# Optimization experiments

Hardware: AMD Instinct MI355X
Metric: run time of the kernel (lower is better)

## Reference

```python
import jax, jax.numpy as jnp
import numpy as np

NUM_HEADS = 16


def setup_inputs() -> dict:
    key = jax.random.key(0)
    ks = jax.random.split(key, 8)
    B, S, D = 2, 2048, 1024
    q = jax.random.normal(ks[0], (B, S, D), dtype=jnp.float32)
    k = jax.random.normal(ks[1], (B, S, D), dtype=jnp.float32)
    v = jax.random.normal(ks[2], (B, S, D), dtype=jnp.float32)
    mask = jax.random.randint(ks[3], (1, 1, S, S), 0, 2, dtype=jnp.int32)
    sc = 1.0 / np.sqrt(D)
    wq = jax.random.normal(ks[4], (D, D), dtype=jnp.float32) * sc
    wk = jax.random.normal(ks[5], (D, D), dtype=jnp.float32) * sc
    wv = jax.random.normal(ks[6], (D, D), dtype=jnp.float32) * sc
    wout = jax.random.normal(ks[7], (D, D), dtype=jnp.float32) * sc
    return {"q": q, "k": k, "v": v, "mask": mask,
            "wq": wq, "wk": wk, "wv": wv, "wout": wout}


def reference(q, k, v, mask, wq, wk, wv, wout):
    B, S, D = q.shape
    H = NUM_HEADS
    hd = D // H

    def proj(x, w):
        # nn.Linear(bias=False): x @ w.T, then split heads -> [B,H,S,hd]
        return (x @ w.T).reshape(B, -1, H, hd).transpose(0, 2, 1, 3)

    qh, kh, vh = proj(q, wq), proj(k, wk), proj(v, wv)
    scale = jnp.asarray(hd, q.dtype) ** 0.5
    scores = jnp.einsum('bhqd,bhkd->bhqk', qh, kh) / scale  # [B,H,S,S]
    att = jax.nn.softmax(scores, axis=-1)
    # NOTE: original applies masked_fill AFTER softmax with value -1e-9
    att = jnp.where(mask == 0, jnp.asarray(-1e-9, att.dtype), att)
    out = jnp.einsum('bhqk,bhkd->bhqd', att, vh)  # [B,H,S,hd]
    out = out.transpose(0, 2, 1, 3).reshape(B, S, D)
    return out @ wout.T
```

## Files before the change

kernel.cpp:

```cpp
#include <hip/hip_runtime.h>
#include <stdint.h>


#define BATCH  2
#define S_LEN  2048
#define DMODEL 1024
#define NH     16
#define HD     64

typedef __bf16 bf16_t;
typedef short  short8 __attribute__((ext_vector_type(8)));
typedef float  f32x4  __attribute__((ext_vector_type(4)));

#define AS1 __attribute__((address_space(1)))
#define AS3 __attribute__((address_space(3)))

static constexpr size_t MB = (size_t)1 << 20;
static constexpr size_t WS_REQUIRED = 112 * MB;
#define OFF_XHI(z)  ((size_t)(z) * 16 * MB)
#define OFF_XLO(z)  (OFF_XHI(z) + 8 * MB)
#define OFF_WHI(z)  (48 * MB + (size_t)(z) * 4 * MB)
#define OFF_WLO(z)  (OFF_WHI(z) + 2 * MB)
#define OFF_PHI(z)  (64 * MB + (size_t)(z) * 16 * MB)
#define OFF_PLO(z)  (OFF_PHI(z) + 8 * MB)
#define OFF_OHI     ((size_t)0)
#define OFF_OLO     (8 * MB)
#define OFF_MASKB   (16 * MB)

__device__ __forceinline__ f32x4 mfma_bf16(short8 a, short8 b, f32x4 c) {
    return __builtin_amdgcn_mfma_f32_16x16x32_bf16(a, b, c, 0, 0, 0);
}

__device__ __forceinline__ short8 ld8(const bf16_t* p) {
    return *reinterpret_cast<const short8*>(p);
}

__global__ void cvt_split_kernel(const float* __restrict__ x,
                                 bf16_t* __restrict__ hi, bf16_t* __restrict__ lo,
                                 int n) {
    int i = (blockIdx.x * blockDim.x + threadIdx.x) * 4;
    if (i >= n) return;
    const float4 v = *reinterpret_cast<const float4*>(x + i);
    float s[4] = {v.x, v.y, v.z, v.w};
    ushort hbits[4], lbits[4];
#pragma unroll
    for (int j = 0; j < 4; j++) {
        bf16_t hh = (bf16_t)s[j];
        bf16_t ll = (bf16_t)(s[j] - (float)hh);
        hbits[j] = __builtin_bit_cast(ushort, hh);
        lbits[j] = __builtin_bit_cast(ushort, ll);
    }
    *reinterpret_cast<ushort4*>(hi + i) = ushort4{hbits[0], hbits[1], hbits[2], hbits[3]};
    *reinterpret_cast<ushort4*>(lo + i) = ushort4{lbits[0], lbits[1], lbits[2], lbits[3]};
}

__global__ void cvt_mask_kernel(const int* __restrict__ m, bf16_t* __restrict__ mb, int n) {
    int i = (blockIdx.x * blockDim.x + threadIdx.x) * 4;
    if (i >= n) return;
    const int4 v = *reinterpret_cast<const int4*>(m + i);
    int s[4] = {v.x, v.y, v.z, v.w};
    ushort b[4];
#pragma unroll
    for (int j = 0; j < 4; j++) {
        bf16_t t = (bf16_t)(s[j] ? 1.0f : 0.0f);
        b[j] = __builtin_bit_cast(ushort, t);
    }
    *reinterpret_cast<ushort4*>(mb + i) = ushort4{b[0], b[1], b[2], b[3]};
}

template <int FINAL>
__global__ __launch_bounds__(256, 2) void gemm_split_kernel(char* __restrict__ ws,
                                                            float* __restrict__ fout) {
    __shared__ __align__(16) bf16_t AsH[128 * 32];
    __shared__ __align__(16) bf16_t AsL[128 * 32];
    __shared__ __align__(16) bf16_t BsH[128 * 32];
    __shared__ __align__(16) bf16_t BsL[128 * 32];

    const int z = FINAL ? 3 : blockIdx.z;
    const bf16_t* Ahi = FINAL ? (const bf16_t*)(ws + OFF_OHI) : (const bf16_t*)(ws + OFF_XHI(z));
    const bf16_t* Alo = FINAL ? (const bf16_t*)(ws + OFF_OLO) : (const bf16_t*)(ws + OFF_XLO(z));
    const bf16_t* Bhi = (const bf16_t*)(ws + OFF_WHI(z));
    const bf16_t* Blo = (const bf16_t*)(ws + OFF_WLO(z));
    bf16_t* Ohi = FINAL ? nullptr : (bf16_t*)(ws + OFF_PHI(z));
    bf16_t* Olo = FINAL ? nullptr : (bf16_t*)(ws + OFF_PLO(z));
    const float scale = (!FINAL && z == 0) ? 0.18033688011112042f : 1.0f;

    const int tid = threadIdx.x;
    const int lane = tid & 63, w = tid >> 6;
    const int wr = w >> 1, wc = w & 1;
    const int fr = lane & 15, fg = lane >> 4;
    const int m0 = blockIdx.x * 128, n0 = blockIdx.y * 128;
    const int K = 1024;

    f32x4 acc[4][4];
#pragma unroll
    for (int i = 0; i < 4; i++)
#pragma unroll
        for (int j = 0; j < 4; j++) acc[i][j] = f32x4{0.f, 0.f, 0.f, 0.f};

    AS3 bf16_t* asAH = (AS3 bf16_t*)AsH;
    AS3 bf16_t* asAL = (AS3 bf16_t*)AsL;
    AS3 bf16_t* asBH = (AS3 bf16_t*)BsH;
    AS3 bf16_t* asBL = (AS3 bf16_t*)BsL;

#pragma unroll 1
    for (int ks = 0; ks < K; ks += 32) {
        __syncthreads();
#pragma unroll
        for (int i = 0; i < 2; i++) {
            const int c = i * 256 + tid;
            const int row = c >> 2;
            const int ce = (c & 3) * 8;
            const size_t gA = (size_t)(m0 + row) * K + ks + ce;
            const size_t gB = (size_t)(n0 + row) * K + ks + ce;
            const size_t d = (size_t)(i * 256 + w * 64) * 8;
            __builtin_amdgcn_global_load_lds((const AS1 void*)(Ahi + gA), (AS3 void*)(asAH + d), 16, 0, 0);
            __builtin_amdgcn_global_load_lds((const AS1 void*)(Alo + gA), (AS3 void*)(asAL + d), 16, 0, 0);
            __builtin_amdgcn_global_load_lds((const AS1 void*)(Bhi + gB), (AS3 void*)(asBH + d), 16, 0, 0);
            __builtin_amdgcn_global_load_lds((const AS1 void*)(Blo + gB), (AS3 void*)(asBL + d), 16, 0, 0);
        }
        __syncthreads();

        short8 afh[4], afl[4], bfh[4], bfl[4];
#pragma unroll
        for (int i = 0; i < 4; i++) {
            const int ao = (wr * 64 + i * 16 + fr) * 32 + fg * 8;
            const int bo = (wc * 64 + i * 16 + fr) * 32 + fg * 8;
            afh[i] = ld8(&AsH[ao]);
            afl[i] = ld8(&AsL[ao]);
            bfh[i] = ld8(&BsH[bo]);
            bfl[i] = ld8(&BsL[bo]);
        }
#pragma unroll
        for (int i = 0; i < 4; i++)
#pragma unroll
            for (int j = 0; j < 4; j++) {
                acc[i][j] = mfma_bf16(afh[i], bfh[j], acc[i][j]);
                acc[i][j] = mfma_bf16(afh[i], bfl[j], acc[i][j]);
                acc[i][j] = mfma_bf16(afl[i], bfh[j], acc[i][j]);
            }
    }

#pragma unroll
    for (int i = 0; i < 4; i++) {
#pragma unroll
        for (int j = 0; j < 4; j++) {
            const int ncol = n0 + wc * 64 + j * 16 + fr;
#pragma unroll
            for (int r = 0; r < 4; r++) {
                const int m = m0 + wr * 64 + i * 16 + fg * 4 + r;
                const float val = acc[i][j][r] * scale;
                if (FINAL) {
                    fout[(size_t)m * DMODEL + ncol] = val;
                } else {
                    const bf16_t h = (bf16_t)val;
                    const bf16_t l = (bf16_t)(val - (float)h);
                    const int b = m >> 11, s = m & (S_LEN - 1);
                    const int hh = ncol >> 6, d = ncol & (HD - 1);
                    size_t idx;
                    if (z == 2) idx = ((size_t)(b * NH + hh) * HD + d) * S_LEN + s;
                    else        idx = ((size_t)(b * NH + hh) * S_LEN + s) * HD + d;
                    Ohi[idx] = h;
                    Olo[idx] = l;
                }
            }
        }
    }
}

__global__ __launch_bounds__(256, 2) void attn_kernel(char* __restrict__ ws) {
    __shared__ __align__(16) bf16_t KsH[2][8 * 64 * 8];
    __shared__ __align__(16) bf16_t KsL[2][8 * 64 * 8];
    __shared__ __align__(16) bf16_t VsH[8 * 64 * 8];
    __shared__ __align__(16) bf16_t VsL[8 * 64 * 8];

    const bf16_t* Qhi = (const bf16_t*)(ws + OFF_PHI(0));
    const bf16_t* Qlo = (const bf16_t*)(ws + OFF_PLO(0));
    const bf16_t* Khi = (const bf16_t*)(ws + OFF_PHI(1));
    const bf16_t* Klo = (const bf16_t*)(ws + OFF_PLO(1));
    const bf16_t* Vhi = (const bf16_t*)(ws + OFF_PHI(2));
    const bf16_t* Vlo = (const bf16_t*)(ws + OFF_PLO(2));
    const bf16_t* Mb  = (const bf16_t*)(ws + OFF_MASKB);
    bf16_t* Ohi = (bf16_t*)(ws + OFF_OHI);
    bf16_t* Olo = (bf16_t*)(ws + OFF_OLO);

    const int tid = threadIdx.x, lane = tid & 63, w = tid >> 6;
    const int fr = lane & 15, fg = lane >> 4;
    const int bh = blockIdx.y;
    const int q0 = blockIdx.x * 128;
    const int qrow0 = q0 + w * 32 + fr;
    const size_t qkBase = (size_t)bh * S_LEN * HD;
    const size_t vtBase = (size_t)bh * HD * S_LEN;

    size_t kSrc[2], vSrc[2];
#pragma unroll
    for (int i = 0; i < 2; i++) {
        const int s = i * 256 + tid;
        const int l = s & 63, f = (s >> 6) & 7;
        const int sfr = l & 15, sfg = l >> 4;
        const int cf = f >> 1, kc = f & 1;
        const int r = (cf & 1) * 4 + (sfr & 3) + (sfr >> 2) * 8 + (cf >> 1) * 32;
        kSrc[i] = qkBase + (size_t)r * HD + kc * 32 + sfg * 8;
        vSrc[i] = vtBase + (size_t)((f >> 1) * 16 + sfr) * S_LEN + (f & 1) * 32 + sfg * 8;
    }

    short8 qh[2][2], ql[2][2];
#pragma unroll
    for (int mf = 0; mf < 2; mf++)
#pragma unroll
        for (int kc = 0; kc < 2; kc++) {
            const size_t off = qkBase + (size_t)(qrow0 + mf * 16) * HD + kc * 32 + fg * 8;
            qh[mf][kc] = ld8(Qhi + off);
            ql[mf][kc] = ld8(Qlo + off);
        }

    f32x4 acco[2][4];
#pragma unroll
    for (int mf = 0; mf < 2; mf++)
#pragma unroll
        for (int df = 0; df < 4; df++) acco[mf][df] = f32x4{0.f, 0.f, 0.f, 0.f};
    float mrun[2] = {-__builtin_inff(), -__builtin_inff()};
    float lrun[2] = {0.f, 0.f};

    const size_t mrowBase0 = (size_t)qrow0 * S_LEN;
    const size_t mrowBase1 = (size_t)(qrow0 + 16) * S_LEN;

#define STAGE_K(K0, BUF)                                                                           \
    {                                                                                              \
        _Pragma("unroll") for (int i = 0; i < 2; i++) {                                            \
            const size_t ko = kSrc[i] + (size_t)(K0) * HD;                                         \
            const size_t dst = (size_t)(i * 256 + w * 64) * 8;                                     \
            __builtin_amdgcn_global_load_lds((const AS1 void*)(Khi + ko),                          \
                                             (AS3 void*)((AS3 bf16_t*)KsH[BUF] + dst), 16, 0, 0);  \
            __builtin_amdgcn_global_load_lds((const AS1 void*)(Klo + ko),                          \
                                             (AS3 void*)((AS3 bf16_t*)KsL[BUF] + dst), 16, 0, 0);  \
        }                                                                                          \
    }
#define STAGE_V(K0)                                                                                \
    {                                                                                              \
        _Pragma("unroll") for (int i = 0; i < 2; i++) {                                            \
            const size_t vo = vSrc[i] + (K0);                                                      \
            const size_t dst = (size_t)(i * 256 + w * 64) * 8;                                     \
            __builtin_amdgcn_global_load_lds((const AS1 void*)(Vhi + vo),                          \
                                             (AS3 void*)((AS3 bf16_t*)VsH + dst), 16, 0, 0);       \
            __builtin_amdgcn_global_load_lds((const AS1 void*)(Vlo + vo),                          \
                                             (AS3 void*)((AS3 bf16_t*)VsL + dst), 16, 0, 0);       \
        }                                                                                          \
    }

    STAGE_K(0, 0)
    short8 mvCur[2][2], mvNxt[2][2];
    mvCur[0][0] = ld8(Mb + mrowBase0 + fg * 8);
    mvCur[0][1] = ld8(Mb + mrowBase0 + 32 + fg * 8);
    mvCur[1][0] = ld8(Mb + mrowBase1 + fg * 8);
    mvCur[1][1] = ld8(Mb + mrowBase1 + 32 + fg * 8);
#pragma unroll
    for (int mf = 0; mf < 2; mf++)
#pragma unroll
        for (int hh = 0; hh < 2; hh++) mvNxt[mf][hh] = mvCur[mf][hh];
    __syncthreads();

    int cur = 0;
#pragma unroll 1
    for (int k0 = 0; k0 < S_LEN; k0 += 64) {
        STAGE_V(k0)
        if (k0 + 64 < S_LEN) {
            STAGE_K(k0 + 64, cur ^ 1)
            mvNxt[0][0] = ld8(Mb + mrowBase0 + (k0 + 64) + fg * 8);
            mvNxt[0][1] = ld8(Mb + mrowBase0 + (k0 + 64) + 32 + fg * 8);
            mvNxt[1][0] = ld8(Mb + mrowBase1 + (k0 + 64) + fg * 8);
            mvNxt[1][1] = ld8(Mb + mrowBase1 + (k0 + 64) + 32 + fg * 8);
        }

        f32x4 sacc[2][4];
#pragma unroll
        for (int mf = 0; mf < 2; mf++)
#pragma unroll
            for (int cf = 0; cf < 4; cf++) sacc[mf][cf] = f32x4{0.f, 0.f, 0.f, 0.f};
        __builtin_amdgcn_s_setprio(1);
#pragma unroll
        for (int cf = 0; cf < 4; cf++) {
#pragma unroll
            for (int kc = 0; kc < 2; kc++) {
                const int fi = cf * 2 + kc;
                const short8 kh = ld8(&KsH[cur][(fi * 64 + lane) * 8]);
                const short8 kl = ld8(&KsL[cur][(fi * 64 + lane) * 8]);
#pragma unroll
                for (int mf = 0; mf < 2; mf++) {
                    sacc[mf][cf] = mfma_bf16(kh, qh[mf][kc], sacc[mf][cf]);
                    sacc[mf][cf] = mfma_bf16(kl, qh[mf][kc], sacc[mf][cf]);
                    sacc[mf][cf] = mfma_bf16(kh, ql[mf][kc], sacc[mf][cf]);
                }
            }
        }
        __builtin_amdgcn_s_setprio(0);

        float p[2][4][4];
#pragma unroll
        for (int mf = 0; mf < 2; mf++) {
            float mx = sacc[mf][0][0];
#pragma unroll
            for (int cf = 0; cf < 4; cf++)
#pragma unroll
                for (int r = 0; r < 4; r++) mx = fmaxf(mx, sacc[mf][cf][r]);
            mx = fmaxf(mx, __shfl_xor(mx, 16, 64));
            mx = fmaxf(mx, __shfl_xor(mx, 32, 64));
            if (!__all(mx <= mrun[mf] + 8.0f)) {
                const float mnew = fmaxf(mrun[mf], mx);
                const float alpha = exp2f(mrun[mf] - mnew);
                mrun[mf] = mnew;
                lrun[mf] *= alpha;
#pragma unroll
                for (int df = 0; df < 4; df++) acco[mf][df] *= alpha;
            }
            float psum = 0.f;
#pragma unroll
            for (int cf = 0; cf < 4; cf++)
#pragma unroll
                for (int r = 0; r < 4; r++) {
                    p[mf][cf][r] = exp2f(sacc[mf][cf][r] - mrun[mf]);
                    psum += p[mf][cf][r];
                }
            psum += __shfl_xor(psum, 16, 64);
            psum += __shfl_xor(psum, 32, 64);
            lrun[mf] += psum;
        }

        short8 phi[2][2], plo[2][2];
#pragma unroll
        for (int mf = 0; mf < 2; mf++)
#pragma unroll
            for (int kc2 = 0; kc2 < 2; kc2++)
#pragma unroll
                for (int j = 0; j < 8; j++) {
                    const int cf = kc2 * 2 + (j >> 2), r = j & 3;
                    const float mvf = (float)__builtin_bit_cast(
                        bf16_t, (ushort)(mvCur[mf][cf >> 1][(cf & 1) * 4 + r]));
                    const float pm = p[mf][cf][r] * mvf;
                    const bf16_t h = (bf16_t)pm;
                    const bf16_t l = (bf16_t)(pm - (float)h);
                    phi[mf][kc2][j] = __builtin_bit_cast(short, h);
                    plo[mf][kc2][j] = __builtin_bit_cast(short, l);
                }

        __syncthreads();

        __builtin_amdgcn_s_setprio(1);
#pragma unroll
        for (int kc2 = 0; kc2 < 2; kc2++) {
#pragma unroll
            for (int df = 0; df < 4; df++) {
                const int fi = df * 2 + kc2;
                const short8 vh = ld8(&VsH[(fi * 64 + lane) * 8]);
                const short8 vl = ld8(&VsL[(fi * 64 + lane) * 8]);
#pragma unroll
                for (int mf = 0; mf < 2; mf++) {
                    acco[mf][df] = mfma_bf16(vh, phi[mf][kc2], acco[mf][df]);
                    acco[mf][df] = mfma_bf16(vl, phi[mf][kc2], acco[mf][df]);
                    acco[mf][df] = mfma_bf16(vh, plo[mf][kc2], acco[mf][df]);
                }
            }
        }
        __builtin_amdgcn_s_setprio(0);

        __syncthreads();
#pragma unroll
        for (int mf = 0; mf < 2; mf++)
#pragma unroll
            for (int hh = 0; hh < 2; hh++) mvCur[mf][hh] = mvNxt[mf][hh];
        cur ^= 1;
    }
#undef STAGE_K
#undef STAGE_V

    const int b = bh >> 4, hh = bh & (NH - 1);
#pragma unroll
    for (int mf = 0; mf < 2; mf++) {
        const float inv = 1.0f / lrun[mf];
        const size_t obase = ((size_t)b * S_LEN + qrow0 + mf * 16) * DMODEL + hh * HD;
#pragma unroll
        for (int df = 0; df < 4; df++) {
#pragma unroll
            for (int r = 0; r < 4; r++) {
                const int d = df * 16 + fg * 4 + r;
                const float o = acco[mf][df][r] * inv;
                const bf16_t h = (bf16_t)o;
                Ohi[obase + d] = h;
                Olo[obase + d] = (bf16_t)(o - (float)h);
            }
        }
    }
}

extern "C" void kernel_launch(void* const* d_in, const int* in_sizes, int n_in,
                              void* d_out, int out_size, void* d_ws, size_t ws_size,
                              hipStream_t stream) {
    (void)in_sizes; (void)n_in; (void)out_size;
    if (ws_size < WS_REQUIRED) return;

    const float* q    = (const float*)d_in[0];
    const float* k    = (const float*)d_in[1];
    const float* v    = (const float*)d_in[2];
    const int*   mask = (const int*)  d_in[3];
    const float* wq   = (const float*)d_in[4];
    const float* wk   = (const float*)d_in[5];
    const float* wv   = (const float*)d_in[6];
    const float* wout = (const float*)d_in[7];
    char* ws = (char*)d_ws;
    float* out = (float*)d_out;

    const size_t nX = (size_t)BATCH * S_LEN * DMODEL;
    const size_t nW = (size_t)DMODEL * DMODEL;
    const size_t nM = (size_t)S_LEN * S_LEN;
    const dim3 blk(256);

    cvt_split_kernel<<<dim3(nX / 1024), blk, 0, stream>>>(q, (bf16_t*)(ws + OFF_XHI(0)), (bf16_t*)(ws + OFF_XLO(0)), (int)nX);
    cvt_split_kernel<<<dim3(nX / 1024), blk, 0, stream>>>(k, (bf16_t*)(ws + OFF_XHI(1)), (bf16_t*)(ws + OFF_XLO(1)), (int)nX);
    cvt_split_kernel<<<dim3(nX / 1024), blk, 0, stream>>>(v, (bf16_t*)(ws + OFF_XHI(2)), (bf16_t*)(ws + OFF_XLO(2)), (int)nX);
    cvt_split_kernel<<<dim3(nW / 1024), blk, 0, stream>>>(wq,   (bf16_t*)(ws + OFF_WHI(0)), (bf16_t*)(ws + OFF_WLO(0)), (int)nW);
    cvt_split_kernel<<<dim3(nW / 1024), blk, 0, stream>>>(wk,   (bf16_t*)(ws + OFF_WHI(1)), (bf16_t*)(ws + OFF_WLO(1)), (int)nW);
    cvt_split_kernel<<<dim3(nW / 1024), blk, 0, stream>>>(wv,   (bf16_t*)(ws + OFF_WHI(2)), (bf16_t*)(ws + OFF_WLO(2)), (int)nW);
    cvt_split_kernel<<<dim3(nW / 1024), blk, 0, stream>>>(wout, (bf16_t*)(ws + OFF_WHI(3)), (bf16_t*)(ws + OFF_WLO(3)), (int)nW);

    gemm_split_kernel<0><<<dim3(32, 8, 3), blk, 0, stream>>>(ws, nullptr);

    cvt_mask_kernel<<<dim3(nM / 1024), blk, 0, stream>>>(mask, (bf16_t*)(ws + OFF_MASKB), (int)nM);

    attn_kernel<<<dim3(S_LEN / 128, BATCH * NH), blk, 0, stream>>>(ws);

    gemm_split_kernel<1><<<dim3(32, 8, 1), blk, 0, stream>>>(ws, out);
}
```

Measured before the change: 419.3 us.

## Double-buffer split-bf16 GEMM LDS tiles and batch conversion launches

```diff
diff --git a/kernel.cpp b/kernel.cpp
--- a/kernel.cpp
+++ b/kernel.cpp
@@ -35,11 +35,10 @@
     return *reinterpret_cast<const short8*>(p);
 }
 
-__global__ void cvt_split_kernel(const float* __restrict__ x,
-                                 bf16_t* __restrict__ hi, bf16_t* __restrict__ lo,
-                                 int n) {
-    int i = (blockIdx.x * blockDim.x + threadIdx.x) * 4;
-    if (i >= n) return;
+__device__ __forceinline__ void cvt_split_body(const float* __restrict__ x,
+                                               bf16_t* __restrict__ hi,
+                                               bf16_t* __restrict__ lo) {
+    const int i = (blockIdx.x * blockDim.x + threadIdx.x) * 4;
     const float4 v = *reinterpret_cast<const float4*>(x + i);
     float s[4] = {v.x, v.y, v.z, v.w};
     ushort hbits[4], lbits[4];
@@ -52,6 +51,21 @@
     }
     *reinterpret_cast<ushort4*>(hi + i) = ushort4{hbits[0], hbits[1], hbits[2], hbits[3]};
     *reinterpret_cast<ushort4*>(lo + i) = ushort4{lbits[0], lbits[1], lbits[2], lbits[3]};
+}
+
+__global__ void cvt_qkv_kernel(const float* __restrict__ q, const float* __restrict__ k,
+                               const float* __restrict__ v, char* __restrict__ ws) {
+    const int z = blockIdx.y;
+    const float* src = (z == 0) ? q : (z == 1) ? k : v;
+    cvt_split_body(src, (bf16_t*)(ws + OFF_XHI(z)), (bf16_t*)(ws + OFF_XLO(z)));
+}
+
+__global__ void cvt_w_kernel(const float* __restrict__ wq, const float* __restrict__ wk,
+                             const float* __restrict__ wv, const float* __restrict__ wout,
+                             char* __restrict__ ws) {
+    const int z = blockIdx.y;
+    const float* src = (z == 0) ? wq : (z == 1) ? wk : (z == 2) ? wv : wout;
+    cvt_split_body(src, (bf16_t*)(ws + OFF_WHI(z)), (bf16_t*)(ws + OFF_WLO(z)));
 }
 
 __global__ void cvt_mask_kernel(const int* __restrict__ m, bf16_t* __restrict__ mb, int n) {
@@ -71,10 +85,10 @@
 template <int FINAL>
 __global__ __launch_bounds__(256, 2) void gemm_split_kernel(char* __restrict__ ws,
                                                             float* __restrict__ fout) {
-    __shared__ __align__(16) bf16_t AsH[128 * 32];
-    __shared__ __align__(16) bf16_t AsL[128 * 32];
-    __shared__ __align__(16) bf16_t BsH[128 * 32];
-    __shared__ __align__(16) bf16_t BsL[128 * 32];
+    __shared__ __align__(16) bf16_t AsH[2][128 * 32];
+    __shared__ __align__(16) bf16_t AsL[2][128 * 32];
+    __shared__ __align__(16) bf16_t BsH[2][128 * 32];
+    __shared__ __align__(16) bf16_t BsL[2][128 * 32];
 
     const int z = FINAL ? 3 : blockIdx.z;
     const bf16_t* Ahi = FINAL ? (const bf16_t*)(ws + OFF_OHI) : (const bf16_t*)(ws + OFF_XHI(z));
@@ -98,39 +112,52 @@
 #pragma unroll
         for (int j = 0; j < 4; j++) acc[i][j] = f32x4{0.f, 0.f, 0.f, 0.f};
 
-    AS3 bf16_t* asAH = (AS3 bf16_t*)AsH;
-    AS3 bf16_t* asAL = (AS3 bf16_t*)AsL;
-    AS3 bf16_t* asBH = (AS3 bf16_t*)BsH;
-    AS3 bf16_t* asBL = (AS3 bf16_t*)BsL;
-
+    size_t gAoff[2], gBoff[2], ldst[2];
+#pragma unroll
+    for (int i = 0; i < 2; i++) {
+        const int c = i * 256 + tid;
+        const int row = c >> 2;
+        const int ce = (c & 3) * 8;
+        gAoff[i] = (size_t)(m0 + row) * K + ce;
+        gBoff[i] = (size_t)(n0 + row) * K + ce;
+        ldst[i] = (size_t)(i * 256 + w * 64) * 8;
+    }
+
+#define GSTAGE(KS, BUF)                                                                            \
+    {                                                                                              \
+        _Pragma("unroll") for (int i = 0; i < 2; i++) {                                            \
+            const size_t gA = gAoff[i] + (KS);                                                     \
+            const size_t gB = gBoff[i] + (KS);                                                     \
+            __builtin_amdgcn_global_load_lds((const AS1 void*)(Ahi + gA),                          \
+                                             (AS3 void*)((AS3 bf16_t*)AsH[BUF] + ldst[i]), 16, 0, 0); \
+            __builtin_amdgcn_global_load_lds((const AS1 void*)(Alo + gA),                          \
+                                             (AS3 void*)((AS3 bf16_t*)AsL[BUF] + ldst[i]), 16, 0, 0); \
+            __builtin_amdgcn_global_load_lds((const AS1 void*)(Bhi + gB),                          \
+                                             (AS3 void*)((AS3 bf16_t*)BsH[BUF] + ldst[i]), 16, 0, 0); \
+            __builtin_amdgcn_global_load_lds((const AS1 void*)(Blo + gB),                          \
+                                             (AS3 void*)((AS3 bf16_t*)BsL[BUF] + ldst[i]), 16, 0, 0); \
+        }                                                                                          \
+    }
+
+    GSTAGE(0, 0)
+    __syncthreads();
+
+    int cur = 0;
 #pragma unroll 1
     for (int ks = 0; ks < K; ks += 32) {
-        __syncthreads();
-#pragma unroll
-        for (int i = 0; i < 2; i++) {
-            const int c = i * 256 + tid;
-            const int row = c >> 2;
-            const int ce = (c & 3) * 8;
-            const size_t gA = (size_t)(m0 + row) * K + ks + ce;
-            const size_t gB = (size_t)(n0 + row) * K + ks + ce;
-            const size_t d = (size_t)(i * 256 + w * 64) * 8;
-            __builtin_amdgcn_global_load_lds((const AS1 void*)(Ahi + gA), (AS3 void*)(asAH + d), 16, 0, 0);
-            __builtin_amdgcn_global_load_lds((const AS1 void*)(Alo + gA), (AS3 void*)(asAL + d), 16, 0, 0);
-            __builtin_amdgcn_global_load_lds((const AS1 void*)(Bhi + gB), (AS3 void*)(asBH + d), 16, 0, 0);
-            __builtin_amdgcn_global_load_lds((const AS1 void*)(Blo + gB), (AS3 void*)(asBL + d), 16, 0, 0);
-        }
-        __syncthreads();
+        if (ks + 32 < K) GSTAGE(ks + 32, cur ^ 1)
 
         short8 afh[4], afl[4], bfh[4], bfl[4];
 #pragma unroll
         for (int i = 0; i < 4; i++) {
             const int ao = (wr * 64 + i * 16 + fr) * 32 + fg * 8;
             const int bo = (wc * 64 + i * 16 + fr) * 32 + fg * 8;
-            afh[i] = ld8(&AsH[ao]);
-            afl[i] = ld8(&AsL[ao]);
-            bfh[i] = ld8(&BsH[bo]);
-            bfl[i] = ld8(&BsL[bo]);
-        }
+            afh[i] = ld8(&AsH[cur][ao]);
+            afl[i] = ld8(&AsL[cur][ao]);
+            bfh[i] = ld8(&BsH[cur][bo]);
+            bfl[i] = ld8(&BsL[cur][bo]);
+        }
+        __builtin_amdgcn_s_setprio(1);
 #pragma unroll
         for (int i = 0; i < 4; i++)
 #pragma unroll
@@ -139,7 +166,12 @@
                 acc[i][j] = mfma_bf16(afh[i], bfl[j], acc[i][j]);
                 acc[i][j] = mfma_bf16(afl[i], bfh[j], acc[i][j]);
             }
-    }
+        __builtin_amdgcn_s_setprio(0);
+
+        __syncthreads();
+        cur ^= 1;
+    }
+#undef GSTAGE
 
 #pragma unroll
     for (int i = 0; i < 4; i++) {
@@ -414,13 +446,8 @@
     const size_t nM = (size_t)S_LEN * S_LEN;
     const dim3 blk(256);
 
-    cvt_split_kernel<<<dim3(nX / 1024), blk, 0, stream>>>(q, (bf16_t*)(ws + OFF_XHI(0)), (bf16_t*)(ws + OFF_XLO(0)), (int)nX);
-    cvt_split_kernel<<<dim3(nX / 1024), blk, 0, stream>>>(k, (bf16_t*)(ws + OFF_XHI(1)), (bf16_t*)(ws + OFF_XLO(1)), (int)nX);
-    cvt_split_kernel<<<dim3(nX / 1024), blk, 0, stream>>>(v, (bf16_t*)(ws + OFF_XHI(2)), (bf16_t*)(ws + OFF_XLO(2)), (int)nX);
-    cvt_split_kernel<<<dim3(nW / 1024), blk, 0, stream>>>(wq,   (bf16_t*)(ws + OFF_WHI(0)), (bf16_t*)(ws + OFF_WLO(0)), (int)nW);
-    cvt_split_kernel<<<dim3(nW / 1024), blk, 0, stream>>>(wk,   (bf16_t*)(ws + OFF_WHI(1)), (bf16_t*)(ws + OFF_WLO(1)), (int)nW);
-    cvt_split_kernel<<<dim3(nW / 1024), blk, 0, stream>>>(wv,   (bf16_t*)(ws + OFF_WHI(2)), (bf16_t*)(ws + OFF_WLO(2)), (int)nW);
-    cvt_split_kernel<<<dim3(nW / 1024), blk, 0, stream>>>(wout, (bf16_t*)(ws + OFF_WHI(3)), (bf16_t*)(ws + OFF_WLO(3)), (int)nW);
+    cvt_qkv_kernel<<<dim3(nX / 1024, 3), blk, 0, stream>>>(q, k, v, ws);
+    cvt_w_kernel<<<dim3(nW / 1024, 4), blk, 0, stream>>>(wq, wk, wv, wout, ws);
 
     gemm_split_kernel<0><<<dim3(32, 8, 3), blk, 0, stream>>>(ws, nullptr);
 
```

After: 411.2 us. About the same (-1.9%).
